# Kernel tuning notes

Measured on AMD Instinct MI355X. Metric: run time of the kernel, lower is better.

The kernel has to match this reference:

```python
import jax, jax.numpy as jnp
import numpy as np

BS, C, H, W = 128, 256, 9, 9
D = 9                      # spectral window size
PS = 15                    # padsize
PAD_SPACE = PS - H         # 6
PAD1 = D // 2              # 4 (spectral pad)
START = PAD_SPACE // 2     # 3 (output crop offset)
SPE_HEAD = 25
SHARE_HEAD = 9
SIDE = 5                   # spe_head_Sidelength
BN_EPS = 1e-5


def setup_inputs() -> dict:
    key = jax.random.key(0)
    ks = jax.random.split(key, 12)
    s = 0.1
    return {
        "x": jax.random.normal(ks[0], (BS, C, H, W), jnp.float32),
        "wk": jax.random.normal(ks[1], (H * W, 1, D), jnp.float32) * s,   # depthwise conv1d over spectral axis
        "bk": jax.random.normal(ks[2], (H * W,), jnp.float32) * s,
        "w1": jax.random.normal(ks[3], (SPE_HEAD, SHARE_HEAD, 2 * SHARE_HEAD), jnp.float32) * s,  # grouped 1x1, no bias
        "bn_gamma": jnp.ones((SPE_HEAD * SHARE_HEAD,), jnp.float32),
        "bn_beta": jnp.zeros((SPE_HEAD * SHARE_HEAD,), jnp.float32),
        "bn_mean": jax.random.normal(ks[4], (SPE_HEAD * SHARE_HEAD,), jnp.float32) * s,
        "bn_var": jax.random.uniform(ks[5], (SPE_HEAD * SHARE_HEAD,), jnp.float32, 0.5, 1.5),
        "w2": jax.random.normal(ks[6], (SPE_HEAD, D, SHARE_HEAD), jnp.float32) * s,  # grouped 1x1 -> spe_head*d
        "b2": jax.random.normal(ks[7], (SPE_HEAD * D,), jnp.float32) * s,
        "wv": jax.random.normal(ks[8], (C, 1, 3, 3), jnp.float32) * s,   # depthwise 3x3
        "bv": jax.random.normal(ks[9], (C,), jnp.float32) * s,
    }


def _unfold_k3_d5(t, bs, c):
    # torch nn.Unfold(kernel=3, dilation=5) on a 15x15 map -> 5x5 output positions.
    # row = kh*5 + oh, col = kw*5 + ow, so a plain (3,5,3,5) reshape gives the taps.
    t = t.reshape(bs, c, 3, SIDE, 3, SIDE)              # (bs,c,kh,oh,kw,ow)
    t = t.transpose(0, 1, 2, 4, 3, 5)                   # (bs,c,kh,kw,oh,ow)
    t = t.reshape(bs, c * SHARE_HEAD, SPE_HEAD)          # (bs, c*9, 25) torch unfold layout
    return t.transpose(0, 2, 1)                          # (bs, 25, c*9)


def reference(x, wk, bk, w1, bn_gamma, bn_beta, bn_mean, bn_var, w2, b2, wv, bv):
    bs, c, h, w = x.shape
    # --- key: depthwise conv1d along spectral (channel) axis, one filter per pixel ---
    k = x.reshape(bs, c, h * w).transpose(0, 2, 1)       # (bs, 81, c)
    k1 = jax.lax.conv_general_dilated(
        k, wk, (1,), [(PAD1, PAD1)],
        dimension_numbers=("NCH", "OIH", "NCH"), feature_group_count=h * w,
    ) + bk[None, :, None]                                # (bs, 81, c)
    k1 = k1.transpose(0, 2, 1).reshape(bs, c, h, w)

    # --- pad right/bottom and unfold q, k ---
    k1_pad = jnp.pad(k1, ((0, 0), (0, 0), (0, PAD_SPACE), (0, PAD_SPACE)))  # (bs,c,15,15)
    q_pad = jnp.pad(x, ((0, 0), (0, 0), (0, PAD_SPACE), (0, PAD_SPACE)))
    key_u = _unfold_k3_d5(k1_pad, bs, c)                 # (bs,25,9c)
    q_u = _unfold_k3_d5(q_pad, bs, c)

    # stack + reshape exactly as torch (row-major): (bs,25,2,9c) -> (bs,450,c)
    key_q = jnp.stack((q_u, key_u), axis=2).reshape(bs, 2 * SPE_HEAD * SHARE_HEAD, c)

    # --- attention_embed: grouped 1x1 conv -> BN(eval) -> ReLU -> grouped 1x1 conv ---
    a = jnp.einsum("goi,bgic->bgoc", w1, key_q.reshape(bs, SPE_HEAD, 2 * SHARE_HEAD, c))
    a = a.reshape(bs, SPE_HEAD * SHARE_HEAD, c)          # (bs,225,c)
    inv_std = bn_gamma / jnp.sqrt(bn_var + BN_EPS)
    a = (a - bn_mean[None, :, None]) * inv_std[None, :, None] + bn_beta[None, :, None]
    a = jax.nn.relu(a)
    a = jnp.einsum("goi,bgic->bgoc", w2, a.reshape(bs, SPE_HEAD, SHARE_HEAD, c))
    a = a.reshape(bs, SPE_HEAD * D, c) + b2[None, :, None]  # (bs,225,c)

    # --- build per-pixel spectral kernels: tile, rearrange to 15x15, softmax over d ---
    att = jnp.tile(a.reshape(bs, SPE_HEAD, D, c), (1, SHARE_HEAD, 1, 1))  # (bs,225,9,c)
    att = att.transpose(0, 3, 1, 2)                      # (bs,c,225,d)
    att = att.reshape(bs, c, 3, 3, SIDE, SIDE, D)
    att = att.transpose(0, 1, 2, 4, 3, 5, 6)             # swap dims 3,4 as torch .transpose(3,4)
    att = att.reshape(bs, c, PS, PS, D)
    att = jax.nn.softmax(att, axis=-1)
    att = att.transpose(0, 1, 4, 2, 3)                   # (bs,c,d,15,15)

    # --- value: depthwise 3x3 conv, pad left/top + spectral, sliding window over channels ---
    v = jax.lax.conv_general_dilated(
        x, wv, (1, 1), [(1, 1), (1, 1)],
        dimension_numbers=("NCHW", "OIHW", "NCHW"), feature_group_count=c,
    ) + bv[None, :, None, None]                          # (bs,c,9,9)
    pv = jnp.pad(v, ((0, 0), (PAD1, PAD1), (PAD_SPACE, 0), (PAD_SPACE, 0)))  # (bs,c+8,15,15)
    v_unf = jnp.stack([pv[:, t:t + c] for t in range(D)], axis=2)            # (bs,c,d,15,15)

    out = jnp.sum(v_unf * att, axis=2) + k1_pad          # (bs,c,15,15)
    return out[:, :, START:h + START, START:w + START]    # (bs,c,9,9)
```

## Files before the change

### kernel.cpp

```cpp
#include <hip/hip_runtime.h>

#define C 256
#define HW 81
#define PITCH 292
#define PITCHD 146
#define ZROW 81

typedef __fp16 h2 __attribute__((ext_vector_type(2)));

__device__ __forceinline__ float us2f(unsigned short u) {
  union { unsigned short s; __fp16 h; } c; c.s = u; return (float)c.h;
}
__device__ __forceinline__ float lo_h(unsigned int d) {
  union { unsigned int i; h2 h; } c; c.i = d; return (float)c.h.x;
}
__device__ __forceinline__ float hi_h(unsigned int d) {
  union { unsigned int i; h2 h; } c; c.i = d; return (float)c.h.y;
}
__device__ __forceinline__ unsigned int pkh2(float a, float b) {
  union { h2 h; unsigned int i; } c;
  c.h = __builtin_amdgcn_cvt_pkrtz(a, b);
  return c.i;
}
__device__ __forceinline__ h2 as_h2(unsigned int d) {
  union { unsigned int i; h2 h; } c; c.i = d; return c.h;
}
__device__ __forceinline__ float dot2(unsigned int a, unsigned int b, float c) {
#if __has_builtin(__builtin_amdgcn_fdot2)
  return __builtin_amdgcn_fdot2(as_h2(a), as_h2(b), c, false);
#else
  h2 x = as_h2(a), y = as_h2(b);
  return fmaf((float)x.y, (float)y.y, fmaf((float)x.x, (float)y.x, c));
#endif
}
__device__ __forceinline__ float exp2_fast(float x) {
#if __has_builtin(__builtin_amdgcn_exp2f)
  return __builtin_amdgcn_exp2f(x);
#else
  return __expf(x * 0.6931471805599453f);
#endif
}

__global__ __launch_bounds__(1024) void semca_fused(
    const float* __restrict__ x, const float* __restrict__ wk,
    const float* __restrict__ bk, const float* __restrict__ w1,
    const float* __restrict__ gamma, const float* __restrict__ beta,
    const float* __restrict__ mean, const float* __restrict__ var,
    const float* __restrict__ w2, const float* __restrict__ b2,
    const float* __restrict__ wv, const float* __restrict__ bv,
    float* __restrict__ out) {
  __shared__ unsigned short xT[82 * PITCH];
  __shared__ unsigned short k1T[82 * PITCH];
  __shared__ unsigned short vT[18 * PITCH];
  __shared__ unsigned short pixtab[228];
  __shared__ float2 bnf[225];
  __shared__ unsigned int w1p[225 * 12];
  __shared__ unsigned int w2p[225 * 4];
  __shared__ uint2 wkp[81 * 3];

  const int blk = blockIdx.x;
  const int b = (blk & 7) * 16 + ((blk >> 3) & 15);
  const int s = blk >> 7;
  const int tid = threadIdx.x;
  const float* xb = x + (size_t)b * (C * HW);

  unsigned int* xTd = (unsigned int*)xT;
  unsigned int* k1Td = (unsigned int*)k1T;
  unsigned int* vTd = (unsigned int*)vT;
  unsigned int* wkpd = (unsigned int*)wkp;

  float xe[11], xo[11];
  int adr[11];
  {
    int chp = tid / HW;
    int p = tid - chp * HW;
#pragma unroll
    for (int rep = 0; rep < 10; ++rep) {
      const float* base = xb + (2 * chp) * HW + p;
      xe[rep] = base[0];
      xo[rep] = base[HW];
      adr[rep] = PITCHD * p + 2 + chp;
      chp += 12;
      p += 52;
      if (p >= HW) { p -= HW; chp += 1; }
    }
    if (tid < 128) {
      int f = 10240 + tid;
      int c2 = f / HW, p2 = f - c2 * HW;
      xe[10] = xb[2 * c2 * HW + p2];
      xo[10] = xb[(2 * c2 + 1) * HW + p2];
      adr[10] = PITCHD * p2 + 2 + c2;
    }
  }

  for (int t = tid; t < 810; t += 1024) {
    int p = t / 10, k2 = t - (t / 10) * 10;
    xT[p * PITCH + ((k2 < 4) ? k2 : (256 + k2))] = 0;
  }
  if (tid < PITCHD) {
    xTd[PITCHD * ZROW + tid] = 0;
    k1Td[PITCHD * ZROW + tid] = 0;
  }
  for (int t = tid; t < 225; t += 1024) {
    int g = t / 9, tap = t - (t / 9) * 9;
    int kh = tap / 3, kw = tap - kh * 3;
    int h = kh * 5 + g / 5, w = kw * 5 + (g - (g / 5) * 5);
    pixtab[t] = (h < 9 && w < 9) ? (unsigned short)((h * 9 + w) * PITCH)
                                 : (unsigned short)(ZROW * PITCH);
    float inv = gamma[t] * rsqrtf(var[t] + 1e-5f);
    bnf[t] = make_float2(inv, beta[t] - mean[t] * inv);
  }
  for (int t = tid; t < 2025; t += 1024) {
    int m = t / 9, q = t - m * 9;
    w1p[m * 12 + q] = pkh2(w1[m * 18 + q], w1[m * 18 + 9 + q]);
  }
  if (tid < 900) {
    int m = tid >> 2, j = tid & 3;
    w2p[m * 4 + j] = pkh2(w2[m * 9 + 2 * j], w2[m * 9 + 2 * j + 1]);
  }
  if (tid < 486) {
    int m = tid / 6, j = tid - (tid / 6) * 6;
    const float* wr = wk + m * 9;
    unsigned int v;
    if (j < 4)       v = pkh2(wr[2 * j], wr[2 * j + 1]);
    else if (j == 4) v = pkh2(wr[8], 0.f);
    else             v = pkh2(0.f, wr[8]);
    wkpd[m * 6 + j] = v;
  }

  const int chv = tid & 127;
  float wv_e[9], wv_o[9];
#pragma unroll
  for (int t = 0; t < 9; ++t) {
    wv_e[t] = wv[(2 * chv) * 9 + t];
    wv_o[t] = wv[(2 * chv + 1) * 9 + t];
  }
  const float bv_e = bv[2 * chv], bv_o = bv[2 * chv + 1];

#pragma unroll
  for (int rep = 0; rep < 10; ++rep) xTd[adr[rep]] = pkh2(xe[rep], xo[rep]);
  if (tid < 128) xTd[adr[10]] = pkh2(xe[10], xo[10]);

  __syncthreads();

  {
    auto k1fn8 = [&](int p, int oct) {
      const uint2* wrow2 = (const uint2*)(xTd + PITCHD * p + 4 * oct);
      uint2 r0 = wrow2[0], r1 = wrow2[1], r2 = wrow2[2], r3 = wrow2[3];
      unsigned int W[8] = {r0.x, r0.y, r1.x, r1.y, r2.x, r2.y, r3.x, r3.y};
      unsigned int A[7];
#pragma unroll
      for (int k2 = 0; k2 < 7; ++k2)
        A[k2] = (W[k2] >> 16) | (W[k2 + 1] << 16);
      const uint2* wkq = wkp + p * 3;
      uint2 wa = wkq[0], wb = wkq[1], wc = wkq[2];
      float bkp = bk[p];
      float cc[8];
#pragma unroll
      for (int j2 = 0; j2 < 4; ++j2) {
        cc[2 * j2] =
            dot2(W[j2], wa.x, dot2(W[j2 + 1], wa.y, dot2(W[j2 + 2], wb.x,
            dot2(W[j2 + 3], wb.y, dot2(W[j2 + 4], wc.x, bkp)))));
        cc[2 * j2 + 1] =
            dot2(A[j2], wa.x, dot2(A[j2 + 1], wa.y, dot2(A[j2 + 2], wb.x,
            dot2(A[j2 + 3], wb.y, dot2(W[j2 + 4], wc.y, bkp)))));
      }
      unsigned int* dst = k1Td + PITCHD * p + 2 + 4 * oct;
      *(uint2*)dst = make_uint2(pkh2(cc[0], cc[1]), pkh2(cc[2], cc[3]));
      *(uint2*)(dst + 2) = make_uint2(pkh2(cc[4], cc[5]), pkh2(cc[6], cc[7]));
    };
    if (s == 0) {
#pragma unroll
      for (int rep = 0; rep < 2; ++rep) {
        int f = tid + rep * 1024;
        k1fn8(9 + (f >> 5), f & 31);
      }
      if (tid < 256) {
        int f = 2048 + tid;
        k1fn8(9 + (f >> 5), f & 31);
      }
    } else {
      auto prow = [&](int f) {
        int idx = f >> 5;
        int ri = idx / 9, col = idx - ri * 9;
        int row = ri + ((ri >= 2) ? 2 : 0);
        return row * 9 + col;
      };
      k1fn8(prow(tid), tid & 31);
      if (tid < 416) {
        int f = 1024 + tid;
        k1fn8(prow(f), f & 31);
      }
    }
  }

  {
    auto vfn = [&](int f) {
      int e = __builtin_amdgcn_readfirstlane(f >> 7);
      int r0 = e / 6;
      int i = s * 3 + r0;
      int j = e - r0 * 6;
      float a_e = bv_e, a_o = bv_o;
#pragma unroll
      for (int di = 0; di < 3; ++di) {
        int ii = i + di - 1;
        if (ii < 0) continue;
#pragma unroll
        for (int dj = 0; dj < 3; ++dj) {
          int jj = j + dj - 1;
          if (jj < 0) continue;
          unsigned int d = xTd[PITCHD * (ii * 9 + jj) + 2 + chv];
          int t = di * 3 + dj;
          a_e = fmaf(lo_h(d), wv_e[t], a_e);
          a_o = fmaf(hi_h(d), wv_o[t], a_o);
        }
      }
      vTd[PITCHD * e + 2 + chv] = pkh2(a_e, a_o);
    };
#pragma unroll
    for (int rep = 0; rep < 2; ++rep) vfn(tid + rep * 1024);
    if (tid < 256) vfn(2048 + tid);
  }
  if (tid < 180) {
    int e = tid / 10, k2 = tid - (tid / 10) * 10;
    vT[e * PITCH + ((k2 < 4) ? k2 : (256 + k2))] = 0;
  }
  __syncthreads();

  const int s4 = tid >> 8;
  const int ch = tid & 255;
  const int ci0 = ch / 9;
  const int tap0 = ch - ci0 * 9;
  float* outb = out + ((size_t)b * C + ch) * HW;

  int tq[9], cq[9];
  {
    int ci = ci0, tap = tap0;
#pragma unroll
    for (int q = 0; q < 9; ++q) {
      tq[q] = tap;
      cq[q] = 4 + ci;
      tap += 4;
      ci += 28;
      if (tap >= 9) { tap -= 9; ci += 1; }
    }
  }

#define PV_STORE(OH, OW)                                                   \
  do {                                                                     \
    int e_ = gh_i * 6 + ((OW)-3);                                          \
    const unsigned short* vrow_ = vT + e_ * PITCH;                         \
    float acc_ = 0.f;                                                      \
    _Pragma("unroll") for (int d_ = 0; d_ < 9; ++d_) acc_ =                \
        fmaf(a2[d_], us2f(vrow_[ch + d_]), acc_);                          \
    if ((OH) < 6 && (OW) < 6)                                              \
      acc_ = fmaf(acc_, inv_s,                                             \
                  us2f(k1T[(((OH) + 3) * 9 + ((OW) + 3)) * PITCH + 4 + ch])); \
    else                                                                   \
      acc_ *= inv_s;                                                       \
    if (valid_inst) outb[(OH)*9 + (OW)] = acc_;                            \
  } while (0)

#pragma unroll
  for (int k = 0; k < 4; ++k) {
    int idx = s4 * 4 + k;
    const bool valid_inst = (idx < 15);
    if (!valid_inst) idx = 14;
    int gh_i = idx / 5, gw_i = idx - (idx / 5) * 5;
    int oh = (s ? 6 : 3) + gh_i;
    int gh = s ? ((gh_i + 4) % 5) : (gh_i + 1);
    int g9 = __builtin_amdgcn_readfirstlane((gh * 5 + gw_i) * 9);

    unsigned int kqp[9];
#pragma unroll
    for (int q = 0; q < 9; ++q) {
      int off = (int)pixtab[g9 + tq[q]] + cq[q];
      unsigned int xv = xT[off], kv = k1T[off];
      kqp[q] = xv | (kv << 16);
    }

    __builtin_amdgcn_s_setprio(1);
    float r[9];
#pragma unroll
    for (int o = 0; o < 9; ++o) {
      int m = g9 + o;
      const unsigned int* wp = w1p + m * 12;
      float a = 0.f;
#pragma unroll
      for (int q = 0; q < 9; ++q) a = dot2(kqp[q], wp[q], a);
      float2 bn = bnf[m];
      a = fmaf(a, bn.x, bn.y);
      r[o] = fmaxf(a, 0.f);
    }

    unsigned int rp[4];
#pragma unroll
    for (int j = 0; j < 4; ++j) rp[j] = pkh2(r[2 * j], r[2 * j + 1]);
    float a2[9], mx = -1e30f;
#pragma unroll
    for (int d = 0; d < 9; ++d) {
      int m = g9 + d;
      const unsigned int* wq = w2p + m * 4;
      float a = b2[m];
#pragma unroll
      for (int j = 0; j < 4; ++j) a = dot2(rp[j], wq[j], a);
      a = fmaf(w2[m * 9 + 8], r[8], a);
      a2[d] = a;
      mx = fmaxf(mx, a);
    }
    const float L2E = 1.44269504f;
    float nmL = mx * -L2E;
    float ssum = 0.f;
#pragma unroll
    for (int d = 0; d < 9; ++d) {
      a2[d] = exp2_fast(fmaf(a2[d], L2E, nmL));
      ssum += a2[d];
    }
    float inv_s = __builtin_amdgcn_rcpf(ssum);
    __builtin_amdgcn_s_setprio(0);

    int ow0 = (gw_i == 0) ? 7 : (gw_i + 2);
    PV_STORE(oh, ow0);
    if (gw_i == 1) PV_STORE(oh, 8);
  }
#undef PV_STORE

  if (s == 0) {
    if (s4 < 3) {
      int oh = s4;
#pragma unroll
      for (int ow = 0; ow < 9; ++ow) {
        float v2 = 0.f;
        if (ow < 6)
          v2 = us2f(k1T[((oh + 3) * 9 + (ow + 3)) * PITCH + 4 + ch]);
        outb[oh * 9 + ow] = v2;
      }
    } else {
#pragma unroll
      for (int r0 = 0; r0 < 3; ++r0) {
        int oh = 3 + r0;
#pragma unroll
        for (int ow = 0; ow < 3; ++ow)
          outb[oh * 9 + ow] =
              us2f(k1T[((oh + 3) * 9 + (ow + 3)) * PITCH + 4 + ch]);
      }
    }
  } else if (s4 < 3) {
    int oh = 6 + s4;
    outb[oh * 9 + 0] = 0.f;
    outb[oh * 9 + 1] = 0.f;
    outb[oh * 9 + 2] = 0.f;
  }
}

extern "C" void kernel_launch(void* const* d_in, const int* in_sizes, int n_in,
                              void* d_out, int out_size, void* d_ws, size_t ws_size,
                              hipStream_t stream) {
  const float* x     = (const float*)d_in[0];
  const float* wk    = (const float*)d_in[1];
  const float* bk    = (const float*)d_in[2];
  const float* w1    = (const float*)d_in[3];
  const float* gamma = (const float*)d_in[4];
  const float* beta  = (const float*)d_in[5];
  const float* mean  = (const float*)d_in[6];
  const float* var   = (const float*)d_in[7];
  const float* w2    = (const float*)d_in[8];
  const float* b2    = (const float*)d_in[9];
  const float* wv    = (const float*)d_in[10];
  const float* bv    = (const float*)d_in[11];
  float* out = (float*)d_out;

  hipLaunchKernelGGL(semca_fused, dim3(256), dim3(1024), 0, stream,
                     x, wk, bk, w1, gamma, beta, mean, var, w2, b2, wv, bv, out);
}
```

Baseline: 25.27 us.

## Rebalance k1 rows and output stores across halves, pack value conv to half2

```diff
diff --git a/kernel.cpp b/kernel.cpp
--- a/kernel.cpp
+++ b/kernel.cpp
@@ -24,6 +24,9 @@
 }
 __device__ __forceinline__ h2 as_h2(unsigned int d) {
   union { unsigned int i; h2 h; } c; c.i = d; return c.h;
+}
+__device__ __forceinline__ unsigned int as_u32(h2 h) {
+  union { h2 h; unsigned int i; } c; c.h = h; return c.i;
 }
 __device__ __forceinline__ float dot2(unsigned int a, unsigned int b, float c) {
 #if __has_builtin(__builtin_amdgcn_fdot2)
@@ -129,13 +132,11 @@
   }
 
   const int chv = tid & 127;
-  float wv_e[9], wv_o[9];
-#pragma unroll
-  for (int t = 0; t < 9; ++t) {
-    wv_e[t] = wv[(2 * chv) * 9 + t];
-    wv_o[t] = wv[(2 * chv + 1) * 9 + t];
-  }
-  const float bv_e = bv[2 * chv], bv_o = bv[2 * chv + 1];
+  unsigned int wvp[9];
+#pragma unroll
+  for (int t = 0; t < 9; ++t)
+    wvp[t] = pkh2(wv[(2 * chv) * 9 + t], wv[(2 * chv + 1) * 9 + t]);
+  const unsigned int bvp = pkh2(bv[2 * chv], bv[2 * chv + 1]);
 
 #pragma unroll
   for (int rep = 0; rep < 10; ++rep) xTd[adr[rep]] = pkh2(xe[rep], xo[rep]);
@@ -169,28 +170,16 @@
       *(uint2*)dst = make_uint2(pkh2(cc[0], cc[1]), pkh2(cc[2], cc[3]));
       *(uint2*)(dst + 2) = make_uint2(pkh2(cc[4], cc[5]), pkh2(cc[6], cc[7]));
     };
-    if (s == 0) {
-#pragma unroll
-      for (int rep = 0; rep < 2; ++rep) {
-        int f = tid + rep * 1024;
-        k1fn8(9 + (f >> 5), f & 31);
-      }
-      if (tid < 256) {
-        int f = 2048 + tid;
-        k1fn8(9 + (f >> 5), f & 31);
-      }
-    } else {
-      auto prow = [&](int f) {
-        int idx = f >> 5;
-        int ri = idx / 9, col = idx - ri * 9;
-        int row = ri + ((ri >= 2) ? 2 : 0);
-        return row * 9 + col;
-      };
-      k1fn8(prow(tid), tid & 31);
-      if (tid < 416) {
-        int f = 1024 + tid;
-        k1fn8(prow(f), f & 31);
-      }
+    auto prow = [&](int f) {
+      int idx = f >> 5;
+      int ri = idx / 9, col = idx - ri * 9;
+      int row = s == 0 ? (ri + ((ri < 3) ? 1 : 3)) : (ri + ((ri >= 2) ? 1 : 0));
+      return row * 9 + col;
+    };
+    k1fn8(prow(tid), tid & 31);
+    if (tid < 704) {
+      int f = 1024 + tid;
+      k1fn8(prow(f), f & 31);
     }
   }
 
@@ -200,7 +189,7 @@
       int r0 = e / 6;
       int i = s * 3 + r0;
       int j = e - r0 * 6;
-      float a_e = bv_e, a_o = bv_o;
+      h2 acc = as_h2(bvp);
 #pragma unroll
       for (int di = 0; di < 3; ++di) {
         int ii = i + di - 1;
@@ -211,11 +200,10 @@
           if (jj < 0) continue;
           unsigned int d = xTd[PITCHD * (ii * 9 + jj) + 2 + chv];
           int t = di * 3 + dj;
-          a_e = fmaf(lo_h(d), wv_e[t], a_e);
-          a_o = fmaf(hi_h(d), wv_o[t], a_o);
+          acc = as_h2(d) * as_h2(wvp[t]) + acc;
         }
       }
-      vTd[PITCHD * e + 2 + chv] = pkh2(a_e, a_o);
+      vTd[PITCHD * e + 2 + chv] = as_u32(acc);
     };
 #pragma unroll
     for (int rep = 0; rep < 2; ++rep) vfn(tid + rep * 1024);
@@ -326,6 +314,17 @@
 #undef PV_STORE
 
   if (s == 0) {
+    if (s4 == 3) {
+#pragma unroll
+      for (int r0 = 0; r0 < 3; ++r0) {
+        int oh = 3 + r0;
+#pragma unroll
+        for (int ow = 0; ow < 3; ++ow)
+          outb[oh * 9 + ow] =
+              us2f(k1T[((oh + 3) * 9 + (ow + 3)) * PITCH + 4 + ch]);
+      }
+    }
+  } else {
     if (s4 < 3) {
       int oh = s4;
 #pragma unroll
@@ -338,18 +337,12 @@
     } else {
 #pragma unroll
       for (int r0 = 0; r0 < 3; ++r0) {
-        int oh = 3 + r0;
-#pragma unroll
-        for (int ow = 0; ow < 3; ++ow)
-          outb[oh * 9 + ow] =
-              us2f(k1T[((oh + 3) * 9 + (ow + 3)) * PITCH + 4 + ch]);
-      }
-    }
-  } else if (s4 < 3) {
-    int oh = 6 + s4;
-    outb[oh * 9 + 0] = 0.f;
-    outb[oh * 9 + 1] = 0.f;
-    outb[oh * 9 + 2] = 0.f;
+        int oh = 6 + r0;
+        outb[oh * 9 + 0] = 0.f;
+        outb[oh * 9 + 1] = 0.f;
+        outb[oh * 9 + 2] = 0.f;
+      }
+    }
   }
 }
 
```

Result: faster. 24.66 us (-2.4%).
